# Optimization experiments

Measured on AMD Instinct MI355X. Metric: run time of the kernel, lower is better.

The kernel has to match this reference:

```python
import jax, jax.numpy as jnp
import numpy as np
from jax import lax

B, S, D, H_HEADS, K, G, E, HID = 2, 1024, 1024, 16, 31, 4, 2, 2048
HD = D // H_HEADS

def _layer_norm(x, g, b, eps=1e-5):
    mu = jnp.mean(x, axis=-1, keepdims=True)
    var = jnp.mean(jnp.square(x - mu), axis=-1, keepdims=True)
    return (x - mu) * lax.rsqrt(var + eps) * g + b

def setup_inputs() -> dict:
    key = jax.random.key(0)
    ks = jax.random.split(key, 16)
    s = 0.02
    return {
        "x": jax.random.normal(ks[0], (B, S, D), jnp.float32),
        "group_ids": jax.random.randint(ks[1], (B, S), 0, G, jnp.int32),
        "cn_g": jnp.ones((D,), jnp.float32), "cn_b": jnp.zeros((D,), jnp.float32),
        "conv_w": jax.random.normal(ks[2], (D, D, K), jnp.float32) * s,
        "conv_b": jnp.zeros((D,), jnp.float32),
        "an_g": jnp.ones((D,), jnp.float32), "an_b": jnp.zeros((D,), jnp.float32),
        "in_w": jax.random.normal(ks[3], (3 * D, D), jnp.float32) * s,
        "in_b": jnp.zeros((3 * D,), jnp.float32),
        "out_w": jax.random.normal(ks[4], (D, D), jnp.float32) * s,
        "out_b": jnp.zeros((D,), jnp.float32),
        "e_w1": jax.random.normal(ks[5], (G, E, D, HID), jnp.float32) * s,
        "e_b1": jnp.zeros((G, E, HID), jnp.float32),
        "e_w2": jax.random.normal(ks[6], (G, E, HID, D), jnp.float32) * s,
        "e_b2": jnp.zeros((G, E, D), jnp.float32),
    }

def reference(x, group_ids, cn_g, cn_b, conv_w, conv_b, an_g, an_b,
              in_w, in_b, out_w, out_b, e_w1, e_b1, e_w2, e_b2):
    # ---- conv block (dropout off: deterministic/eval) ----
    residual = x
    h = _layer_norm(x, cn_g, cn_b)
    hc = jnp.transpose(h, (0, 2, 1))  # [B, D, S]
    hc = lax.conv_general_dilated(hc, conv_w, window_strides=(1,),
                                  padding=[(K // 2, K // 2)],
                                  dimension_numbers=("NCH", "OIH", "NCH"))
    hc = hc + conv_b[None, :, None]
    hc = jnp.transpose(hc, (0, 2, 1))
    x = jax.nn.gelu(hc, approximate=False) + residual
    # ---- self-attention block ----
    residual = x
    h = _layer_norm(x, an_g, an_b)
    qkv = h @ in_w.T + in_b  # [B, S, 3D]
    q, k, v = jnp.split(qkv, 3, axis=-1)
    q = q.reshape(B, S, H_HEADS, HD)
    k = k.reshape(B, S, H_HEADS, HD)
    v = v.reshape(B, S, H_HEADS, HD)
    scores = jnp.einsum("bqhd,bkhd->bhqk", q, k) / jnp.sqrt(jnp.float32(HD))
    attn = jax.nn.softmax(scores, axis=-1)
    ctx = jnp.einsum("bhqk,bkhd->bqhd", attn, v).reshape(B, S, D)
    x = ctx @ out_w.T + out_b + residual
    # ---- group-routed MoE (dense compute over groups, select by group id) ----
    residual = x
    xf = x.reshape(B * S, D)
    gid = group_ids.reshape(B * S)
    h1 = jax.nn.gelu(jnp.einsum("nd,gedh->ngeh", xf, e_w1) + e_b1, approximate=False)
    out_all = jnp.einsum("ngeh,gehd->nged", h1, e_w2) + e_b2  # [N, G, E, D]
    out_all = jnp.mean(out_all, axis=2)  # mean over experts in group -> [N, G, D]
    sel = jnp.take_along_axis(out_all, gid[:, None, None].astype(jnp.int32), axis=1)[:, 0]
    x = sel.reshape(B, S, D) + residual
    return x
```

## Files before the change

### kernel.cpp

```cpp
#include <hip/hip_runtime.h>
#include <hip/hip_bf16.h>
#include <math.h>

#define BB 2
#define SS 1024
#define DD 1024
#define HH 16
#define HDIM 64
#define KK 31
#define GG 4
#define EE 2
#define HIDN 2048
#define NTOK (BB*SS)
#define D3 (3*DD)

typedef unsigned short u16;
typedef __attribute__((ext_vector_type(8))) short s16x8;
typedef __attribute__((ext_vector_type(8))) unsigned short u16x8;
typedef __attribute__((ext_vector_type(4))) unsigned short u16x4;
typedef __attribute__((ext_vector_type(4))) float f32x4;
typedef __attribute__((ext_vector_type(2))) unsigned int u32x2;

__device__ __forceinline__ float gelu_f(float x) {
  return 0.5f * x * (1.0f + erff(x * 0.7071067811865475f));
}
__device__ __forceinline__ u16 f2bf(float f) {
  unsigned u = __builtin_bit_cast(unsigned, f);
  u = (u + 0x7fffu + ((u >> 16) & 1u)) >> 16;
  return (u16)u;
}
__device__ __forceinline__ float bf2f(u16 u) {
  return __builtin_bit_cast(float, ((unsigned)u) << 16);
}
__device__ __forceinline__ f32x4 MFMA16(s16x8 a, s16x8 b, f32x4 c) {
  return __builtin_amdgcn_mfma_f32_16x16x32_bf16(a, b, c, 0, 0, 0);
}
#define GLOAD16(gp, lp) __builtin_amdgcn_global_load_lds( \
    (const __attribute__((address_space(1))) void*)(gp),  \
    (__attribute__((address_space(3))) void*)(lp), 16, 0, 0)

__global__ void ln_kernel(const float* __restrict__ x, const float* __restrict__ g,
                          const float* __restrict__ b, u16* __restrict__ out) {
  const int row = blockIdx.x;
  const int tid = threadIdx.x;
  __shared__ float red[4];
  const float4 v = reinterpret_cast<const float4*>(x + (size_t)row * DD)[tid];
  float s = v.x + v.y + v.z + v.w;
  s += __shfl_down(s, 32); s += __shfl_down(s, 16); s += __shfl_down(s, 8);
  s += __shfl_down(s, 4);  s += __shfl_down(s, 2);  s += __shfl_down(s, 1);
  if ((tid & 63) == 0) red[tid >> 6] = s;
  __syncthreads();
  const float mean = (red[0] + red[1] + red[2] + red[3]) * (1.0f / DD);
  __syncthreads();
  const float4 d = make_float4(v.x - mean, v.y - mean, v.z - mean, v.w - mean);
  float sq = d.x*d.x + d.y*d.y + d.z*d.z + d.w*d.w;
  sq += __shfl_down(sq, 32); sq += __shfl_down(sq, 16); sq += __shfl_down(sq, 8);
  sq += __shfl_down(sq, 4);  sq += __shfl_down(sq, 2);  sq += __shfl_down(sq, 1);
  if ((tid & 63) == 0) red[tid >> 6] = sq;
  __syncthreads();
  const float var = (red[0] + red[1] + red[2] + red[3]) * (1.0f / DD);
  const float rstd = rsqrtf(var + 1e-5f);
  const float4 gv = reinterpret_cast<const float4*>(g)[tid];
  const float4 bv = reinterpret_cast<const float4*>(b)[tid];
  u16x4 o;
  o[0] = f2bf(d.x * rstd * gv.x + bv.x);
  o[1] = f2bf(d.y * rstd * gv.y + bv.y);
  o[2] = f2bf(d.z * rstd * gv.z + bv.z);
  o[3] = f2bf(d.w * rstd * gv.w + bv.w);
  *reinterpret_cast<u16x4*>(out + (size_t)row * DD + tid * 4) = o;
}

__global__ void prep_convw(const float* __restrict__ cw, u16* __restrict__ Wb) {
  const int o = blockIdx.x;
#pragma unroll
  for (int rep = 0; rep < 4; ++rep) {
    const int i = rep * 256 + threadIdx.x;
    const float* src = cw + ((size_t)o * DD + i) * KK;
    float wv[KK];
#pragma unroll
    for (int k = 0; k < KK; ++k) wv[k] = src[k];
#pragma unroll
    for (int k = 0; k < KK; ++k)
      Wb[((size_t)k * DD + o) * DD + i] = f2bf(wv[k]);
  }
}

__global__ void cvt_kernel(const float* __restrict__ in, u16* __restrict__ outp, int n4) {
  const int i = blockIdx.x * 256 + threadIdx.x;
  if (i < n4) {
    const float4 v = reinterpret_cast<const float4*>(in)[i];
    u16x4 o; o[0] = f2bf(v.x); o[1] = f2bf(v.y); o[2] = f2bf(v.z); o[3] = f2bf(v.w);
    reinterpret_cast<u16x4*>(outp)[i] = o;
  }
}

__global__ void tr_kernel(const float* __restrict__ src, u16* __restrict__ dst, int R, int C) {
  __shared__ float tile[32][33];
  const int c0 = blockIdx.x * 32, r0 = blockIdx.y * 32;
  const size_t base = (size_t)blockIdx.z * R * C;
  const int tx = threadIdx.x & 31, ty = threadIdx.x >> 5;
#pragma unroll
  for (int i = 0; i < 4; ++i)
    tile[ty + i * 8][tx] = src[base + (size_t)(r0 + ty + i * 8) * C + c0 + tx];
  __syncthreads();
#pragma unroll
  for (int i = 0; i < 4; ++i)
    dst[base + (size_t)(c0 + ty + i * 8) * R + r0 + tx] = f2bf(tile[tx][ty + i * 8]);
}

__global__ void vtr_kernel(const u16* __restrict__ qkvb, u16* __restrict__ Vt) {
  __shared__ u16 tile[32][40];
  const int k0 = blockIdx.x * 32, d0 = blockIdx.y * 32, bh = blockIdx.z;
  const int b = bh >> 4, h = bh & 15;
  const int tx = threadIdx.x & 31, ty = threadIdx.x >> 5;
#pragma unroll
  for (int i = 0; i < 4; ++i)
    tile[ty + i * 8][tx] =
        qkvb[(size_t)(b * SS + k0 + ty + i * 8) * D3 + 2 * DD + h * HDIM + d0 + tx];
  __syncthreads();
#pragma unroll
  for (int i = 0; i < 4; ++i)
    Vt[((size_t)(b * HH + h) * HDIM + d0 + ty + i * 8) * SS + k0 + tx] = tile[tx][ty + i * 8];
}

__global__ __launch_bounds__(512) void conv_kernel(const u16* __restrict__ hb,
                                                   const u16* __restrict__ Wb,
                                                   u16* __restrict__ P) {
  const int L = blockIdx.x;
  const int o_t = L & 7;
  const int rest = L >> 3;
  const int s_t = rest >> 1;
  const int z = rest & 1;
  const int b = s_t >> 3, sloc = s_t & 7;
  const int s0l = sloc * 128;
  const int o0 = o_t * 128;
  const int ibase = z * 512;
  const int tid = threadIdx.x, lane = tid & 63, w = tid >> 6;
  const int wm = (w >> 2) & 1, wn = (w >> 1) & 1, ksid = w & 1;
  const int q15 = lane & 15, g = lane >> 4;
  __shared__ __align__(16) u16 Ad[2][160 * 64];
  __shared__ __align__(16) u16 Bp[8][3][2048];
  const int rlo = (sloc == 0) ? 15 : 0;
  const int rhi = (sloc == 7) ? 143 : 158;
  if (sloc == 0)
    for (int i = tid; i < 15 * 64; i += 512) { Ad[0][i] = 0; Ad[1][i] = 0; }
  if (sloc == 7)
    for (int i = tid; i < 17 * 64; i += 512) { Ad[0][143 * 64 + i] = 0; Ad[1][143 * 64 + i] = 0; }
  auto stageA = [&](int buf, int i0) {
    for (int q = w; q < 20; q += 8) {
      const int r = q * 8 + (lane >> 3);
      const int c = (lane & 7) ^ (r & 7);
      if (r >= rlo && r < rhi)
        GLOAD16(hb + (size_t)(b * SS + s0l - 15 + r) * DD + i0 + c * 8, &Ad[buf][q * 512]);
    }
  };
  auto stageBp = [&](int slot, int k, int i0w) {
#pragma unroll
    for (int q = 0; q < 4; ++q) {
      const int j = lane >> 2;
      const int r = q * 16 + j;
      const int c16 = (lane & 3) ^ ((j >> 1) & 3);
      GLOAD16(Wb + ((size_t)k * DD + o0 + wn * 64 + r) * DD + i0w + c16 * 8,
              &Bp[w][slot][q * 512]);
    }
  };
  f32x4 acc[4][4];
#pragma unroll
  for (int i = 0; i < 4; ++i)
#pragma unroll
    for (int j = 0; j < 4; ++j) acc[i][j] = f32x4{0.f, 0.f, 0.f, 0.f};
  const int ib0 = ibase + ksid * 32;
  stageA(0, ibase);
  stageBp(0, 0, ib0);
  stageBp(1, 1, ib0);
  asm volatile("s_waitcnt vmcnt(0)" ::: "memory");
  __syncthreads();
  const int T = 8 * KK;
  const int kx = ksid * 64;
  const int bro = q15 * 64 + ((g ^ ((q15 >> 1) & 3)) << 4);
  int t = 0;
  for (int i0i = 0; i0i < 8; ++i0i) {
    const u16* Ab = Ad[i0i & 1];
    for (int k = 0; k < KK; ++k, ++t) {
      {
        const int tn = t + 2;
        if (tn < T) stageBp(tn % 3, tn % KK, ibase + (tn / KK) * 64 + ksid * 32);
      }
      s16x8 af[4];
      const int rk0 = wm * 64 + q15 + k;
#pragma unroll
      for (int mf = 0; mf < 4; ++mf) {
        const int rr = rk0 + mf * 16;
        const char* p = (const char*)Ab + rr * 128;
        af[mf] = *(const s16x8*)(p + (((g ^ (rr & 7)) * 16) ^ kx));
      }
      if (t + 2 < T)      asm volatile("s_waitcnt vmcnt(8)" ::: "memory");
      else if (t + 1 < T) asm volatile("s_waitcnt vmcnt(4)" ::: "memory");
      else                asm volatile("s_waitcnt vmcnt(0)" ::: "memory");
      if (k == 5 && i0i < 7) stageA((i0i + 1) & 1, ibase + (i0i + 1) * 64);
      const char* Bb = (const char*)&Bp[w][t % 3][0];
      s16x8 bfr[4];
#pragma unroll
      for (int nf = 0; nf < 4; ++nf)
        bfr[nf] = *(const s16x8*)(Bb + nf * 1024 + bro);
      __builtin_amdgcn_s_setprio(1);
#pragma unroll
      for (int mf = 0; mf < 4; ++mf)
#pragma unroll
        for (int nf = 0; nf < 4; ++nf)
          acc[mf][nf] = MFMA16(af[mf], bfr[nf], acc[mf][nf]);
      __builtin_amdgcn_s_setprio(0);
    }
    if (i0i < 7) {
      asm volatile("s_waitcnt vmcnt(0)" ::: "memory");
      __syncthreads();
    }
  }
  __syncthreads();
  float* scr = (float*)(&Bp[0][0][0]) + (wm * 2 + wn) * 4096;
  if (ksid == 1) {
#pragma unroll
    for (int mf = 0; mf < 4; ++mf)
#pragma unroll
      for (int nf = 0; nf < 4; ++nf) {
        const int col = nf * 16 + q15;
        *(f32x4*)&scr[col * 64 + ((mf * 16 + g * 4) ^ ((col & 7) << 3))] = acc[mf][nf];
      }
  }
  __syncthreads();
  if (ksid == 0) {
    u16* Pz = P + (size_t)z * NTOK * DD;
#pragma unroll
    for (int mf = 0; mf < 4; ++mf) {
      f32x4 sum[4];
#pragma unroll
      for (int nf = 0; nf < 4; ++nf) {
        const int col = nf * 16 + q15;
        const f32x4 o = *(const f32x4*)&scr[col * 64 + ((mf * 16 + g * 4) ^ ((col & 7) << 3))];
        sum[nf] = acc[mf][nf] + o;
      }
#pragma unroll
      for (int r = 0; r < 4; ++r) {
        const int srow = s0l + wm * 64 + mf * 16 + g * 4 + r;
        u16* orow = Pz + (size_t)(b * SS + srow) * DD + o0 + wn * 64;
#pragma unroll
        for (int nf = 0; nf < 4; ++nf)
          orow[nf * 16 + q15] = f2bf(sum[nf][r]);
      }
    }
  }
}

__global__ void combine_kernel(const u16* __restrict__ P, const float* __restrict__ cb,
                               const float* __restrict__ x, float* __restrict__ x1) {
  const int idx = blockIdx.x * 256 + threadIdx.x;
  const size_t base = (size_t)idx * 4;
  const int col = (int)(base & (DD - 1));
  const u16x4 p0 = *(const u16x4*)(P + base);
  const u16x4 p1 = *(const u16x4*)(P + (size_t)NTOK * DD + base);
  const float4 xv = *(const float4*)(x + base);
  const float4 cbv = *(const float4*)(cb + col);
  float4 o;
  o.x = gelu_f(bf2f(p0[0]) + bf2f(p1[0]) + cbv.x) + xv.x;
  o.y = gelu_f(bf2f(p0[1]) + bf2f(p1[1]) + cbv.y) + xv.y;
  o.z = gelu_f(bf2f(p0[2]) + bf2f(p1[2]) + cbv.z) + xv.z;
  o.w = gelu_f(bf2f(p0[3]) + bf2f(p1[3]) + cbv.w) + xv.w;
  *(float4*)(x1 + base) = o;
}

__global__ __launch_bounds__(256) void qkv_kernel(const u16* __restrict__ A, const u16* __restrict__ B,
                           const float* __restrict__ bias, u16* __restrict__ C) {
  const int n0 = blockIdx.x * 64, m0 = blockIdx.y * 128;
  const int tid = threadIdx.x, lane = tid & 63, w = tid >> 6;
  const int wm = w >> 1, wn = w & 1;
  __shared__ u16 As[2][128 * 64];
  __shared__ u16 Bs[2][64 * 64];
  f32x4 acc[4][2];
#pragma unroll
  for (int i = 0; i < 4; ++i)
#pragma unroll
    for (int j = 0; j < 2; ++j) acc[i][j] = f32x4{0.f, 0.f, 0.f, 0.f};
  auto stage = [&](int t, int buf) {
    const int k0 = t * 64;
#pragma unroll
    for (int q = 0; q < 4; ++q) {
      const int idx = w * 4 + q, r = idx * 8 + (lane >> 3), c = (lane & 7) ^ (r & 7);
      GLOAD16(A + (size_t)(m0 + r) * DD + k0 + c * 8, &As[buf][idx * 512]);
    }
#pragma unroll
    for (int q = 0; q < 2; ++q) {
      const int idx = w * 2 + q, r = idx * 8 + (lane >> 3), c = (lane & 7) ^ (r & 7);
      GLOAD16(B + (size_t)(n0 + r) * DD + k0 + c * 8, &Bs[buf][idx * 512]);
    }
  };
  stage(0, 0);
  asm volatile("s_waitcnt vmcnt(0)" ::: "memory");
  __syncthreads();
  const int T = DD / 64;
  for (int t = 0; t < T; ++t) {
    if (t + 1 < T) stage(t + 1, (t + 1) & 1);
    const u16* Ab = As[t & 1];
    const u16* Bb = Bs[t & 1];
    const int xb = (((lane >> 4) ^ (lane & 7)) * 16);
    s16x8 af[4][2], bfr[2][2];
#pragma unroll
    for (int mf = 0; mf < 4; ++mf) {
      const char* p = (const char*)Ab + (wm * 64 + mf * 16 + (lane & 15)) * 128;
      af[mf][0] = *(const s16x8*)(p + xb);
      af[mf][1] = *(const s16x8*)(p + (xb ^ 64));
    }
#pragma unroll
    for (int nf = 0; nf < 2; ++nf) {
      const char* p = (const char*)Bb + (wn * 32 + nf * 16 + (lane & 15)) * 128;
      bfr[nf][0] = *(const s16x8*)(p + xb);
      bfr[nf][1] = *(const s16x8*)(p + (xb ^ 64));
    }
#pragma unroll
    for (int ks = 0; ks < 2; ++ks)
#pragma unroll
      for (int mf = 0; mf < 4; ++mf)
#pragma unroll
        for (int nf = 0; nf < 2; ++nf)
          acc[mf][nf] = MFMA16(af[mf][ks], bfr[nf][ks], acc[mf][nf]);
    asm volatile("s_waitcnt vmcnt(0)" ::: "memory");
    __syncthreads();
  }
#pragma unroll
  for (int mf = 0; mf < 4; ++mf)
#pragma unroll
    for (int rr = 0; rr < 4; ++rr) {
      const int row = m0 + wm * 64 + mf * 16 + (lane >> 4) * 4 + rr;
#pragma unroll
      for (int nf = 0; nf < 2; ++nf) {
        const int col = n0 + wn * 32 + nf * 16 + (lane & 15);
        C[(size_t)row * D3 + col] = f2bf(acc[mf][nf][rr] + bias[col]);
      }
    }
}

__global__ __launch_bounds__(256) void out_kernel(const u16* __restrict__ A, const u16* __restrict__ B,
                           const float* __restrict__ bias, const float* __restrict__ resid,
                           float* __restrict__ C, u16* __restrict__ x2g,
                           const int* __restrict__ inv) {
  const int n0 = blockIdx.x * 64, m0 = blockIdx.y * 128;
  const int tid = threadIdx.x, lane = tid & 63, w = tid >> 6;
  const int wm = w >> 1, wn = w & 1;
  __shared__ u16 As[2][128 * 64];
  __shared__ u16 Bs[2][64 * 64];
  f32x4 acc[4][2];
#pragma unroll
  for (int i = 0; i < 4; ++i)
#pragma unroll
    for (int j = 0; j < 2; ++j) acc[i][j] = f32x4{0.f, 0.f, 0.f, 0.f};
  auto stage = [&](int t, int buf) {
    const int k0 = t * 64;
#pragma unroll
    for (int q = 0; q < 4; ++q) {
      const int idx = w * 4 + q, r = idx * 8 + (lane >> 3), c = (lane & 7) ^ (r & 7);
      GLOAD16(A + (size_t)(m0 + r) * DD + k0 + c * 8, &As[buf][idx * 512]);
    }
#pragma unroll
    for (int q = 0; q < 2; ++q) {
      const int idx = w * 2 + q, r = idx * 8 + (lane >> 3), c = (lane & 7) ^ (r & 7);
      GLOAD16(B + (size_t)(n0 + r) * DD + k0 + c * 8, &Bs[buf][idx * 512]);
    }
  };
  stage(0, 0);
  asm volatile("s_waitcnt vmcnt(0)" ::: "memory");
  __syncthreads();
  const int T = DD / 64;
  for (int t = 0; t < T; ++t) {
    if (t + 1 < T) stage(t + 1, (t + 1) & 1);
    const u16* Ab = As[t & 1];
    const u16* Bb = Bs[t & 1];
    const int xb = (((lane >> 4) ^ (lane & 7)) * 16);
    s16x8 af[4][2], bfr[2][2];
#pragma unroll
    for (int mf = 0; mf < 4; ++mf) {
      const char* p = (const char*)Ab + (wm * 64 + mf * 16 + (lane & 15)) * 128;
      af[mf][0] = *(const s16x8*)(p + xb);
      af[mf][1] = *(const s16x8*)(p + (xb ^ 64));
    }
#pragma unroll
    for (int nf = 0; nf < 2; ++nf) {
      const char* p = (const char*)Bb + (wn * 32 + nf * 16 + (lane & 15)) * 128;
      bfr[nf][0] = *(const s16x8*)(p + xb);
      bfr[nf][1] = *(const s16x8*)(p + (xb ^ 64));
    }
#pragma unroll
    for (int ks = 0; ks < 2; ++ks)
#pragma unroll
      for (int mf = 0; mf < 4; ++mf)
#pragma unroll
        for (int nf = 0; nf < 2; ++nf)
          acc[mf][nf] = MFMA16(af[mf][ks], bfr[nf][ks], acc[mf][nf]);
    asm volatile("s_waitcnt vmcnt(0)" ::: "memory");
    __syncthreads();
  }
#pragma unroll
  for (int mf = 0; mf < 4; ++mf)
#pragma unroll
    for (int rr = 0; rr < 4; ++rr) {
      const int row = m0 + wm * 64 + mf * 16 + (lane >> 4) * 4 + rr;
      const int slot = inv[row];
#pragma unroll
      for (int nf = 0; nf < 2; ++nf) {
        const int col = n0 + wn * 32 + nf * 16 + (lane & 15);
        const float v = acc[mf][nf][rr] + bias[col] + resid[(size_t)row * DD + col];
        C[(size_t)row * DD + col] = v;
        x2g[(size_t)slot * DD + col] = f2bf(v);
      }
    }
}

__global__ __launch_bounds__(512) void attn_kernel(const u16* __restrict__ qkv,
                                                   const u16* __restrict__ Vt,
                                                   u16* __restrict__ ctx) {
  const int q0 = blockIdx.x * 128, h = blockIdx.y, b = blockIdx.z;
  const int tid = threadIdx.x, lane = tid & 63, w = tid >> 6;
  const int q15 = lane & 15, g = lane >> 4, l7 = lane & 7;
  __shared__ u16 Q_lds[128 * 64];
  __shared__ u16 K_lds[2][64 * 64];
  __shared__ u16 V_lds[2][64 * 64];
  __shared__ u16 P_lds[8][16 * 72];
  __shared__ float s_lds[8][16];

#pragma unroll
  for (int q2 = 0; q2 < 2; ++q2) {
    const int idx = w * 2 + q2;
    const int r = idx * 8 + (lane >> 3);
    const int c = l7 ^ (r & 7);
    GLOAD16(qkv + (size_t)(b * SS + q0 + r) * D3 + h * HDIM + c * 8, &Q_lds[idx * 512]);
  }
  auto stageK = [&](int buf, int kt) {
    const int r = w * 8 + (lane >> 3);
    const int c = l7 ^ (r & 7);
    GLOAD16(qkv + (size_t)(b * SS + kt * 64 + r) * D3 + DD + h * HDIM + c * 8,
            &K_lds[buf][w * 512]);
  };
  auto stageV = [&](int buf, int kt) {
    const int r = w * 8 + (lane >> 3);
    const int c = l7 ^ (r & 7);
    GLOAD16(Vt + ((size_t)(b * HH + h) * HDIM + r) * SS + kt * 64 + c * 8,
            &V_lds[buf][w * 512]);
  };
  stageK(0, 0);
  stageV(0, 0);
  asm volatile("s_waitcnt vmcnt(0)" ::: "memory");
  __syncthreads();
  s16x8 bq[2];
#pragma unroll
  for (int ks = 0; ks < 2; ++ks)
    bq[ks] = *(const s16x8*)((const char*)Q_lds + (w * 16 + q15) * 128 + ((4 * ks + g) ^ l7) * 16);
  f32x4 oacc[4];
#pragma unroll
  for (int nf = 0; nf < 4; ++nf) oacc[nf] = f32x4{0.f, 0.f, 0.f, 0.f};
  float mrun = -3.0e38f, lrun = 0.0f;
  int buf = 0;
  for (int kt = 0; kt < 16; ++kt) {
    if (kt < 15) { stageK(buf ^ 1, kt + 1); stageV(buf ^ 1, kt + 1); }
    f32x4 st[4];
#pragma unroll
    for (int mf = 0; mf < 4; ++mf) st[mf] = f32x4{0.f, 0.f, 0.f, 0.f};
#pragma unroll
    for (int ks = 0; ks < 2; ++ks) {
#pragma unroll
      for (int mf = 0; mf < 4; ++mf) {
        const s16x8 ka = *(const s16x8*)((const char*)K_lds[buf] + (mf * 16 + q15) * 128 +
                                         ((4 * ks + g) ^ l7) * 16);
        st[mf] = MFMA16(ka, bq[ks], st[mf]);
      }
    }
    float t0[4][4];
    float cmax = -3.0e38f;
#pragma unroll
    for (int mf = 0; mf < 4; ++mf)
#pragma unroll
      for (int r = 0; r < 4; ++r) {
        const float v = st[mf][r] * 0.125f;
        t0[mf][r] = v;
        cmax = fmaxf(cmax, v);
      }
    cmax = fmaxf(cmax, __shfl_xor(cmax, 16));
    cmax = fmaxf(cmax, __shfl_xor(cmax, 32));
    const float mnew = fmaxf(mrun, cmax);
    const float scf = __expf(mrun - mnew);
    float psum = 0.f;
#pragma unroll
    for (int mf = 0; mf < 4; ++mf)
#pragma unroll
      for (int r = 0; r < 4; ++r) {
        const float p = __expf(t0[mf][r] - mnew);
        t0[mf][r] = p;
        psum += p;
      }
    psum += __shfl_xor(psum, 16);
    psum += __shfl_xor(psum, 32);
    lrun = lrun * scf + psum;
    mrun = mnew;
    s_lds[w][q15] = scf;
    u16* pw = &P_lds[w][0];
#pragma unroll
    for (int mf = 0; mf < 4; ++mf) {
      u32x2 pk;
      pk[0] = (unsigned)f2bf(t0[mf][0]) | ((unsigned)f2bf(t0[mf][1]) << 16);
      pk[1] = (unsigned)f2bf(t0[mf][2]) | ((unsigned)f2bf(t0[mf][3]) << 16);
      *(u32x2*)(pw + q15 * 72 + mf * 16 + g * 4) = pk;
    }
    asm volatile("s_waitcnt lgkmcnt(0)" ::: "memory");
    const f32x4 scv = *(const f32x4*)&s_lds[w][g * 4];
#pragma unroll
    for (int nf = 0; nf < 4; ++nf)
#pragma unroll
      for (int r = 0; r < 4; ++r) oacc[nf][r] *= scv[r];
#pragma unroll
    for (int ks = 0; ks < 2; ++ks) {
      const s16x8 pa = *(const s16x8*)(pw + q15 * 72 + ks * 32 + g * 8);
#pragma unroll
      for (int nf = 0; nf < 4; ++nf) {
        const s16x8 bv = *(const s16x8*)((const char*)V_lds[buf] + (nf * 16 + q15) * 128 +
                                         ((4 * ks + g) ^ l7) * 16);
        oacc[nf] = MFMA16(pa, bv, oacc[nf]);
      }
    }
    asm volatile("s_waitcnt vmcnt(0)" ::: "memory");
    __syncthreads();
    buf ^= 1;
  }
  const float linv = 1.0f / lrun;
  s_lds[w][q15] = linv;
  asm volatile("s_waitcnt lgkmcnt(0)" ::: "memory");
  const f32x4 lv = *(const f32x4*)&s_lds[w][g * 4];
#pragma unroll
  for (int nf = 0; nf < 4; ++nf)
#pragma unroll
    for (int r = 0; r < 4; ++r) {
      const int qg = q0 + w * 16 + g * 4 + r;
      ctx[(size_t)(b * SS + qg) * DD + h * HDIM + nf * 16 + q15] = f2bf(oacc[nf][r] * lv[r]);
    }
}

__global__ void zero_counts_kernel(int* c) { if (threadIdx.x < GG) c[threadIdx.x] = 0; }

__global__ void gather_kernel(const int* __restrict__ gid, int* __restrict__ counts,
                              int* __restrict__ gather) {
  const int n = blockIdx.x * 256 + threadIdx.x;
  if (n < NTOK) {
    const int g = gid[n];
    const int slot = atomicAdd(&counts[g], 1);
    gather[g * NTOK + slot] = n;
  }
}

__global__ void scan_kernel(const int* __restrict__ cnts, int* __restrict__ off) {
  if (threadIdx.x == 0) {
    int s = 0;
#pragma unroll
    for (int g = 0; g < GG; ++g) { off[g] = s; s += cnts[g]; }
    off[GG] = s;
  }
}

__global__ void pack_kernel(const int* __restrict__ gat, const int* __restrict__ cnts,
                            const int* __restrict__ off, int* __restrict__ gidx,
                            int* __restrict__ inv) {
  const int g = blockIdx.y;
  const int slot = blockIdx.x * 256 + threadIdx.x;
  if (slot < cnts[g]) {
    const int tok = gat[g * NTOK + slot];
    const int sg = off[g] + slot;
    gidx[sg] = tok;
    inv[tok] = sg;
  }
}

__global__ __launch_bounds__(256) void moe1_kernel(const u16* __restrict__ x2g, const u16* __restrict__ w1t,
                            const float* __restrict__ e_b1, const int* __restrict__ off,
                            const int* __restrict__ cnts, u16* __restrict__ h1) {
  const int ge = blockIdx.z, g = ge >> 1, e = ge & 1;
  const int cnt = cnts[g];
  const int m0 = blockIdx.y * 128;
  if (m0 >= cnt) return;
  const int base = off[g];
  const int n0 = blockIdx.x * 64;
  const u16* A = x2g + (size_t)base * DD;
  const u16* B = w1t + (size_t)ge * HIDN * DD;
  const int tid = threadIdx.x, lane = tid & 63, w = tid >> 6;
  const int wm = w >> 1, wn = w & 1;
  __shared__ u16 As[2][128 * 64];
  __shared__ u16 Bs[2][64 * 64];
  f32x4 acc[4][2];
#pragma unroll
  for (int i = 0; i < 4; ++i)
#pragma unroll
    for (int j = 0; j < 2; ++j) acc[i][j] = f32x4{0.f, 0.f, 0.f, 0.f};
  auto stage = [&](int t, int buf) {
    const int k0 = t * 64;
#pragma unroll
    for (int q = 0; q < 4; ++q) {
      const int idx = w * 4 + q, r = idx * 8 + (lane >> 3), c = (lane & 7) ^ (r & 7);
      int rg = m0 + r; if (rg > cnt - 1) rg = cnt - 1;
      GLOAD16(A + (size_t)rg * DD + k0 + c * 8, &As[buf][idx * 512]);
    }
#pragma unroll
    for (int q = 0; q < 2; ++q) {
      const int idx = w * 2 + q, r = idx * 8 + (lane >> 3), c = (lane & 7) ^ (r & 7);
      GLOAD16(B + (size_t)(n0 + r) * DD + k0 + c * 8, &Bs[buf][idx * 512]);
    }
  };
  stage(0, 0);
  asm volatile("s_waitcnt vmcnt(0)" ::: "memory");
  __syncthreads();
  const int T = DD / 64;
  for (int t = 0; t < T; ++t) {
    if (t + 1 < T) stage(t + 1, (t + 1) & 1);
    const u16* Ab = As[t & 1];
    const u16* Bb = Bs[t & 1];
    const int xb = (((lane >> 4) ^ (lane & 7)) * 16);
    s16x8 af[4][2], bfr[2][2];
#pragma unroll
    for (int mf = 0; mf < 4; ++mf) {
      const char* p = (const char*)Ab + (wm * 64 + mf * 16 + (lane & 15)) * 128;
      af[mf][0] = *(const s16x8*)(p + xb);
      af[mf][1] = *(const s16x8*)(p + (xb ^ 64));
    }
#pragma unroll
    for (int nf = 0; nf < 2; ++nf) {
      const char* p = (const char*)Bb + (wn * 32 + nf * 16 + (lane & 15)) * 128;
      bfr[nf][0] = *(const s16x8*)(p + xb);
      bfr[nf][1] = *(const s16x8*)(p + (xb ^ 64));
    }
#pragma unroll
    for (int ks = 0; ks < 2; ++ks)
#pragma unroll
      for (int mf = 0; mf < 4; ++mf)
#pragma unroll
        for (int nf = 0; nf < 2; ++nf)
          acc[mf][nf] = MFMA16(af[mf][ks], bfr[nf][ks], acc[mf][nf]);
    asm volatile("s_waitcnt vmcnt(0)" ::: "memory");
    __syncthreads();
  }
  const float* b1 = e_b1 + (size_t)ge * HIDN;
#pragma unroll
  for (int mf = 0; mf < 4; ++mf)
#pragma unroll
    for (int rr = 0; rr < 4; ++rr) {
      const int rowg = m0 + wm * 64 + mf * 16 + (lane >> 4) * 4 + rr;
      if (rowg < cnt) {
        u16* orow = h1 + ((size_t)e * NTOK + base + rowg) * HIDN;
#pragma unroll
        for (int nf = 0; nf < 2; ++nf) {
          const int col = n0 + wn * 32 + nf * 16 + (lane & 15);
          orow[col] = f2bf(gelu_f(acc[mf][nf][rr] + b1[col]));
        }
      }
    }
}

__global__ __launch_bounds__(256) void moe2_kernel(const u16* __restrict__ h1, const u16* __restrict__ w2t,
                            const float* __restrict__ e_b2, const int* __restrict__ off,
                            const int* __restrict__ cnts, const int* __restrict__ gidx,
                            const float* __restrict__ x2, float* __restrict__ outp) {
  const int g = blockIdx.z;
  const int cnt = cnts[g];
  const int m0 = blockIdx.y * 128;
  if (m0 >= cnt) return;
  const int base = off[g];
  const int n0 = blockIdx.x * 64;
  const int tid = threadIdx.x, lane = tid & 63, w = tid >> 6;
  const int wm = w >> 1, wn = w & 1;
  __shared__ u16 As[2][128 * 64];
  __shared__ u16 Bs[2][64 * 64];
  f32x4 acc[4][2];
#pragma unroll
  for (int i = 0; i < 4; ++i)
#pragma unroll
    for (int j = 0; j < 2; ++j) acc[i][j] = f32x4{0.f, 0.f, 0.f, 0.f};
  auto stage = [&](int t, int buf) {
    const int e = t >> 5;
    const int k0 = (t & 31) * 64;
#pragma unroll
    for (int q = 0; q < 4; ++q) {
      const int idx = w * 4 + q, r = idx * 8 + (lane >> 3), c = (lane & 7) ^ (r & 7);
      int rg = m0 + r; if (rg > cnt - 1) rg = cnt - 1;
      GLOAD16(h1 + ((size_t)e * NTOK + base + rg) * HIDN + k0 + c * 8, &As[buf][idx * 512]);
    }
#pragma unroll
    for (int q = 0; q < 2; ++q) {
      const int idx = w * 2 + q, r = idx * 8 + (lane >> 3), c = (lane & 7) ^ (r & 7);
      GLOAD16(w2t + ((size_t)(g * EE + e) * DD + n0 + r) * HIDN + k0 + c * 8, &Bs[buf][idx * 512]);
    }
  };
  stage(0, 0);
  asm volatile("s_waitcnt vmcnt(0)" ::: "memory");
  __syncthreads();
  const int T = 64;
  for (int t = 0; t < T; ++t) {
    if (t + 1 < T) stage(t + 1, (t + 1) & 1);
    const u16* Ab = As[t & 1];
    const u16* Bb = Bs[t & 1];
    const int xb = (((lane >> 4) ^ (lane & 7)) * 16);
    s16x8 af[4][2], bfr[2][2];
#pragma unroll
    for (int mf = 0; mf < 4; ++mf) {
      const char* p = (const char*)Ab + (wm * 64 + mf * 16 + (lane & 15)) * 128;
      af[mf][0] = *(const s16x8*)(p + xb);
      af[mf][1] = *(const s16x8*)(p + (xb ^ 64));
    }
#pragma unroll
    for (int nf = 0; nf < 2; ++nf) {
      const char* p = (const char*)Bb + (wn * 32 + nf * 16 + (lane & 15)) * 128;
      bfr[nf][0] = *(const s16x8*)(p + xb);
      bfr[nf][1] = *(const s16x8*)(p + (xb ^ 64));
    }
#pragma unroll
    for (int ks = 0; ks < 2; ++ks)
#pragma unroll
      for (int mf = 0; mf < 4; ++mf)
#pragma unroll
        for (int nf = 0; nf < 2; ++nf)
          acc[mf][nf] = MFMA16(af[mf][ks], bfr[nf][ks], acc[mf][nf]);
    asm volatile("s_waitcnt vmcnt(0)" ::: "memory");
    __syncthreads();
  }
  const float* b20 = e_b2 + (size_t)(g * EE + 0) * DD;
  const float* b21 = e_b2 + (size_t)(g * EE + 1) * DD;
#pragma unroll
  for (int mf = 0; mf < 4; ++mf)
#pragma unroll
    for (int rr = 0; rr < 4; ++rr) {
      const int rowg = m0 + wm * 64 + mf * 16 + (lane >> 4) * 4 + rr;
      if (rowg < cnt) {
        const int tok = gidx[base + rowg];
#pragma unroll
        for (int nf = 0; nf < 2; ++nf) {
          const int col = n0 + wn * 32 + nf * 16 + (lane & 15);
          outp[(size_t)tok * DD + col] =
              0.5f * acc[mf][nf][rr] + 0.5f * (b20[col] + b21[col]) + x2[(size_t)tok * DD + col];
        }
      }
    }
}

extern "C" void kernel_launch(void* const* d_in, const int* in_sizes, int n_in,
                              void* d_out, int out_size, void* d_ws, size_t ws_size,
                              hipStream_t stream) {
  (void)in_sizes; (void)n_in; (void)out_size; (void)ws_size;
  const float* x      = (const float*)d_in[0];
  const int*   gid    = (const int*)d_in[1];
  const float* cn_g   = (const float*)d_in[2];
  const float* cn_b   = (const float*)d_in[3];
  const float* conv_w = (const float*)d_in[4];
  const float* conv_b = (const float*)d_in[5];
  const float* an_g   = (const float*)d_in[6];
  const float* an_b   = (const float*)d_in[7];
  const float* in_w   = (const float*)d_in[8];
  const float* in_b   = (const float*)d_in[9];
  const float* out_w  = (const float*)d_in[10];
  const float* out_b  = (const float*)d_in[11];
  const float* e_w1   = (const float*)d_in[12];
  const float* e_b1   = (const float*)d_in[13];
  const float* e_w2   = (const float*)d_in[14];
  const float* e_b2   = (const float*)d_in[15];
  float* outp = (float*)d_out;

  char* wsp = (char*)d_ws;
  u16*   hb    = (u16*)(wsp);
  u16*   Pc    = (u16*)(wsp + (4ull << 20));
  float* x1    = (float*)(wsp + (12ull << 20));
  u16*   Wb    = (u16*)(wsp + (12ull << 20));
  u16*   qkvb  = (u16*)(wsp + (24ull << 20));
  u16*   inwb  = (u16*)(wsp + (40ull << 20));
  u16*   outwb = (u16*)(wsp + (40ull << 20));
  u16*   Vt    = (u16*)(wsp + (46ull << 20));
  u16*   ctxb  = hb;
  float* x2    = (float*)(wsp + (52ull << 20));
  int*   inv   = (int*)(wsp + (60ull << 20));
  u16*   x2g   = (u16*)(wsp + (64ull << 20));
  u16*   wgt   = (u16*)(wsp + (4ull << 20));
  u16*   h1    = (u16*)(wsp + (36ull << 20));
  int*   gat   = (int*)(wsp + (74ull << 20));
  int*   cnts  = gat + GG * NTOK;
  int*   offp  = cnts + GG;
  int*   gidx  = offp + (GG + 1);

  ln_kernel<<<NTOK, 256, 0, stream>>>(x, cn_g, cn_b, hb);
  prep_convw<<<1024, 256, 0, stream>>>(conv_w, Wb);
  conv_kernel<<<256, 512, 0, stream>>>(hb, Wb, Pc);
  combine_kernel<<<NTOK * DD / 1024, 256, 0, stream>>>(Pc, conv_b, x, x1);
  zero_counts_kernel<<<1, 64, 0, stream>>>(cnts);
  gather_kernel<<<NTOK / 256, 256, 0, stream>>>(gid, cnts, gat);
  scan_kernel<<<1, 64, 0, stream>>>(cnts, offp);
  pack_kernel<<<dim3(NTOK / 256, GG), 256, 0, stream>>>(gat, cnts, offp, gidx, inv);
  ln_kernel<<<NTOK, 256, 0, stream>>>(x1, an_g, an_b, hb);
  cvt_kernel<<<3072, 256, 0, stream>>>(in_w, inwb, 3 * DD * DD / 4);
  qkv_kernel<<<dim3(D3 / 64, NTOK / 128), 256, 0, stream>>>(hb, inwb, in_b, qkvb);
  vtr_kernel<<<dim3(SS / 32, HDIM / 32, BB * HH), 256, 0, stream>>>(qkvb, Vt);
  attn_kernel<<<dim3(SS / 128, HH, BB), 512, 0, stream>>>(qkvb, Vt, ctxb);
  cvt_kernel<<<1024, 256, 0, stream>>>(out_w, outwb, DD * DD / 4);
  out_kernel<<<dim3(DD / 64, NTOK / 128), 256, 0, stream>>>(ctxb, outwb, out_b, x1, x2, x2g, inv);
  tr_kernel<<<dim3(HIDN / 32, DD / 32, GG * EE), 256, 0, stream>>>(e_w1, wgt, DD, HIDN);
  moe1_kernel<<<dim3(HIDN / 64, NTOK / 128, GG * EE), 256, 0, stream>>>(x2g, wgt, e_b1, offp, cnts, h1);
  tr_kernel<<<dim3(DD / 32, HIDN / 32, GG * EE), 256, 0, stream>>>(e_w2, wgt, HIDN, DD);
  moe2_kernel<<<dim3(DD / 64, NTOK / 128, GG), 256, 0, stream>>>(h1, wgt, e_b2, offp, cnts, gidx, x2, outp);
}
```

Baseline: 493.6 us.

## Triple-buffer GEMM shared-memory staging with partial vmcnt waits and MFMA priority

```diff
diff --git a/kernel.cpp b/kernel.cpp
--- a/kernel.cpp
+++ b/kernel.cpp
@@ -273,8 +273,8 @@
   const int n0 = blockIdx.x * 64, m0 = blockIdx.y * 128;
   const int tid = threadIdx.x, lane = tid & 63, w = tid >> 6;
   const int wm = w >> 1, wn = w & 1;
-  __shared__ u16 As[2][128 * 64];
-  __shared__ u16 Bs[2][64 * 64];
+  __shared__ u16 As[3][128 * 64];
+  __shared__ u16 Bs[3][64 * 64];
   f32x4 acc[4][2];
 #pragma unroll
   for (int i = 0; i < 4; ++i)
@@ -294,13 +294,16 @@
     }
   };
   stage(0, 0);
-  asm volatile("s_waitcnt vmcnt(0)" ::: "memory");
-  __syncthreads();
+  stage(1, 1);
   const int T = DD / 64;
   for (int t = 0; t < T; ++t) {
-    if (t + 1 < T) stage(t + 1, (t + 1) & 1);
-    const u16* Ab = As[t & 1];
-    const u16* Bb = Bs[t & 1];
+    if (t + 1 < T) asm volatile("s_waitcnt vmcnt(6)" ::: "memory");
+    else           asm volatile("s_waitcnt vmcnt(0)" ::: "memory");
+    __builtin_amdgcn_s_barrier();
+    asm volatile("" ::: "memory");
+    if (t + 2 < T) stage(t + 2, (t + 2) % 3);
+    const u16* Ab = As[t % 3];
+    const u16* Bb = Bs[t % 3];
     const int xb = (((lane >> 4) ^ (lane & 7)) * 16);
     s16x8 af[4][2], bfr[2][2];
 #pragma unroll
@@ -315,6 +318,7 @@
       bfr[nf][0] = *(const s16x8*)(p + xb);
       bfr[nf][1] = *(const s16x8*)(p + (xb ^ 64));
     }
+    __builtin_amdgcn_s_setprio(1);
 #pragma unroll
     for (int ks = 0; ks < 2; ++ks)
 #pragma unroll
@@ -322,8 +326,7 @@
 #pragma unroll
         for (int nf = 0; nf < 2; ++nf)
           acc[mf][nf] = MFMA16(af[mf][ks], bfr[nf][ks], acc[mf][nf]);
-    asm volatile("s_waitcnt vmcnt(0)" ::: "memory");
-    __syncthreads();
+    __builtin_amdgcn_s_setprio(0);
   }
 #pragma unroll
   for (int mf = 0; mf < 4; ++mf)
@@ -345,8 +348,8 @@
   const int n0 = blockIdx.x * 64, m0 = blockIdx.y * 128;
   const int tid = threadIdx.x, lane = tid & 63, w = tid >> 6;
   const int wm = w >> 1, wn = w & 1;
-  __shared__ u16 As[2][128 * 64];
-  __shared__ u16 Bs[2][64 * 64];
+  __shared__ u16 As[3][128 * 64];
+  __shared__ u16 Bs[3][64 * 64];
   f32x4 acc[4][2];
 #pragma unroll
   for (int i = 0; i < 4; ++i)
@@ -366,13 +369,16 @@
     }
   };
   stage(0, 0);
-  asm volatile("s_waitcnt vmcnt(0)" ::: "memory");
-  __syncthreads();
+  stage(1, 1);
   const int T = DD / 64;
   for (int t = 0; t < T; ++t) {
-    if (t + 1 < T) stage(t + 1, (t + 1) & 1);
-    const u16* Ab = As[t & 1];
-    const u16* Bb = Bs[t & 1];
+    if (t + 1 < T) asm volatile("s_waitcnt vmcnt(6)" ::: "memory");
+    else           asm volatile("s_waitcnt vmcnt(0)" ::: "memory");
+    __builtin_amdgcn_s_barrier();
+    asm volatile("" ::: "memory");
+    if (t + 2 < T) stage(t + 2, (t + 2) % 3);
+    const u16* Ab = As[t % 3];
+    const u16* Bb = Bs[t % 3];
     const int xb = (((lane >> 4) ^ (lane & 7)) * 16);
     s16x8 af[4][2], bfr[2][2];
 #pragma unroll
@@ -387,6 +393,7 @@
       bfr[nf][0] = *(const s16x8*)(p + xb);
       bfr[nf][1] = *(const s16x8*)(p + (xb ^ 64));
     }
+    __builtin_amdgcn_s_setprio(1);
 #pragma unroll
     for (int ks = 0; ks < 2; ++ks)
 #pragma unroll
@@ -394,8 +401,7 @@
 #pragma unroll
         for (int nf = 0; nf < 2; ++nf)
           acc[mf][nf] = MFMA16(af[mf][ks], bfr[nf][ks], acc[mf][nf]);
-    asm volatile("s_waitcnt vmcnt(0)" ::: "memory");
-    __syncthreads();
+    __builtin_amdgcn_s_setprio(0);
   }
 #pragma unroll
   for (int mf = 0; mf < 4; ++mf)
@@ -587,8 +593,8 @@
   const u16* B = w1t + (size_t)ge * HIDN * DD;
   const int tid = threadIdx.x, lane = tid & 63, w = tid >> 6;
   const int wm = w >> 1, wn = w & 1;
-  __shared__ u16 As[2][128 * 64];
-  __shared__ u16 Bs[2][64 * 64];
+  __shared__ u16 As[3][128 * 64];
+  __shared__ u16 Bs[3][64 * 64];
   f32x4 acc[4][2];
 #pragma unroll
   for (int i = 0; i < 4; ++i)
@@ -609,13 +615,16 @@
     }
   };
   stage(0, 0);
-  asm volatile("s_waitcnt vmcnt(0)" ::: "memory");
-  __syncthreads();
+  stage(1, 1);
   const int T = DD / 64;
   for (int t = 0; t < T; ++t) {
-    if (t + 1 < T) stage(t + 1, (t + 1) & 1);
-    const u16* Ab = As[t & 1];
-    const u16* Bb = Bs[t & 1];
+    if (t + 1 < T) asm volatile("s_waitcnt vmcnt(6)" ::: "memory");
+    else           asm volatile("s_waitcnt vmcnt(0)" ::: "memory");
+    __builtin_amdgcn_s_barrier();
+    asm volatile("" ::: "memory");
+    if (t + 2 < T) stage(t + 2, (t + 2) % 3);
+    const u16* Ab = As[t % 3];
+    const u16* Bb = Bs[t % 3];
     const int xb = (((lane >> 4) ^ (lane & 7)) * 16);
     s16x8 af[4][2], bfr[2][2];
 #pragma unroll
@@ -630,6 +639,7 @@
       bfr[nf][0] = *(const s16x8*)(p + xb);
       bfr[nf][1] = *(const s16x8*)(p + (xb ^ 64));
     }
+    __builtin_amdgcn_s_setprio(1);
 #pragma unroll
     for (int ks = 0; ks < 2; ++ks)
 #pragma unroll
@@ -637,8 +647,7 @@
 #pragma unroll
         for (int nf = 0; nf < 2; ++nf)
           acc[mf][nf] = MFMA16(af[mf][ks], bfr[nf][ks], acc[mf][nf]);
-    asm volatile("s_waitcnt vmcnt(0)" ::: "memory");
-    __syncthreads();
+    __builtin_amdgcn_s_setprio(0);
   }
   const float* b1 = e_b1 + (size_t)ge * HIDN;
 #pragma unroll
@@ -669,8 +678,8 @@
   const int n0 = blockIdx.x * 64;
   const int tid = threadIdx.x, lane = tid & 63, w = tid >> 6;
   const int wm = w >> 1, wn = w & 1;
-  __shared__ u16 As[2][128 * 64];
-  __shared__ u16 Bs[2][64 * 64];
+  __shared__ u16 As[3][128 * 64];
+  __shared__ u16 Bs[3][64 * 64];
   f32x4 acc[4][2];
 #pragma unroll
   for (int i = 0; i < 4; ++i)
@@ -692,13 +701,16 @@
     }
   };
   stage(0, 0);
-  asm volatile("s_waitcnt vmcnt(0)" ::: "memory");
-  __syncthreads();
+  stage(1, 1);
   const int T = 64;
   for (int t = 0; t < T; ++t) {
-    if (t + 1 < T) stage(t + 1, (t + 1) & 1);
-    const u16* Ab = As[t & 1];
-    const u16* Bb = Bs[t & 1];
+    if (t + 1 < T) asm volatile("s_waitcnt vmcnt(6)" ::: "memory");
+    else           asm volatile("s_waitcnt vmcnt(0)" ::: "memory");
+    __builtin_amdgcn_s_barrier();
+    asm volatile("" ::: "memory");
+    if (t + 2 < T) stage(t + 2, (t + 2) % 3);
+    const u16* Ab = As[t % 3];
+    const u16* Bb = Bs[t % 3];
     const int xb = (((lane >> 4) ^ (lane & 7)) * 16);
     s16x8 af[4][2], bfr[2][2];
 #pragma unroll
@@ -713,6 +725,7 @@
       bfr[nf][0] = *(const s16x8*)(p + xb);
       bfr[nf][1] = *(const s16x8*)(p + (xb ^ 64));
     }
+    __builtin_amdgcn_s_setprio(1);
 #pragma unroll
     for (int ks = 0; ks < 2; ++ks)
 #pragma unroll
@@ -720,8 +733,7 @@
 #pragma unroll
         for (int nf = 0; nf < 2; ++nf)
           acc[mf][nf] = MFMA16(af[mf][ks], bfr[nf][ks], acc[mf][nf]);
-    asm volatile("s_waitcnt vmcnt(0)" ::: "memory");
-    __syncthreads();
+    __builtin_amdgcn_s_setprio(0);
   }
   const float* b20 = e_b2 + (size_t)(g * EE + 0) * DD;
   const float* b21 = e_b2 + (size_t)(g * EE + 1) * DD;
```

New measurement: 493.1 us. No clear change (-0.1%).
